# Kernel optimization log

Hardware: AMD Instinct MI355X
Metric: run time of the kernel (lower is better)

The kernel has to match this reference:

```python
import jax, jax.numpy as jnp
import numpy as np


def _cofactor_antieq(M):
    """ith output = M[...,i,0] * (-1)**i * det(M with row i and col 0 deleted).

    M: (..., n, n) -> (..., n). Vectorized form of the original per-row
    jnp.delete + stack + det construction.
    """
    n = M.shape[-1]
    # rows[i] = all row indices except i, shape (n, n-1)
    rows = np.stack([np.delete(np.arange(n), i) for i in range(n)])
    Msub = M[..., 1:]                 # delete first column: (..., n, n-1)
    sub = Msub[..., rows, :]          # delete row i per output: (..., n, n-1, n-1)
    signs = jnp.asarray((-1.0) ** np.arange(n), dtype=M.dtype)
    return M[..., 0] * signs * jnp.linalg.det(sub)


def setup_inputs() -> dict:
    key = jax.random.key(0)
    ks = jax.random.split(key, 6)
    B, NSPIN, NPS, D, NION, DIM = 4096, 2, 16, 256, 8, 3
    eq_inputs = jax.random.normal(ks[0], (B, NSPIN * NPS, D), jnp.float32)
    r_ei = jax.random.normal(ks[1], (B, NSPIN * NPS, NION, DIM), jnp.float32)
    # per-spin linear orbital params (stacked over spin since splits are equal)
    W = jax.random.normal(ks[2], (NSPIN, D, NPS), jnp.float32) / np.sqrt(D)
    b = jax.random.normal(ks[3], (NSPIN, NPS), jnp.float32) * 0.01
    # anisotropic envelope decay matrices A per (spin, ion, orbital), near identity
    env_dim = jax.random.normal(ks[4], (NSPIN, NION, NPS, DIM, DIM), jnp.float32) * 0.1 + jnp.eye(DIM, dtype=jnp.float32)
    # linear combination over ions per (spin, orbital)
    env_ion = jax.random.normal(ks[5], (NSPIN, NION, NPS), jnp.float32) / NION
    return dict(eq_inputs=eq_inputs, r_ei=r_ei, W=W, b=b, env_dim=env_dim, env_ion=env_ion)


def reference(eq_inputs, r_ei, W, b, env_dim, env_ion):
    B = eq_inputs.shape[0]
    nspin, d, nps = W.shape
    nion, dim = r_ei.shape[-2], r_ei.shape[-1]
    # split particles by spin: (B, nspin, nps, ...)
    xs = eq_inputs.reshape(B, nspin, nps, d)
    rs = r_ei.reshape(B, nspin, nps, nion, dim)
    # linear part of orbitals: (B, s, n, o) with n = o = nps (square per spin)
    y = jnp.einsum('bsnd,sdo->bsno', xs, W) + b[:, None, :]
    # anisotropic exponential envelope: exp(-||A (r - R)||), summed over ions
    Ar = jnp.einsum('sioed,bsnid->bsnioe', env_dim, rs)        # (B,s,n,ion,orb,3)
    env = jnp.einsum('bsnio,sio->bsno',
                     jnp.exp(-jnp.linalg.norm(Ar, axis=-1)), env_ion)
    M = y * env                                                 # (B, s, n, n)
    cof = _cofactor_antieq(M)                                   # (B, s, n)
    return cof[..., None]                                       # (B, s, n, 1)
```

## Files before the change

### kernel.cpp

```cpp
#include <hip/hip_runtime.h>
#include <math.h>


__global__ __launch_bounds__(256)
void cof_fused(const float* __restrict__ eq,
               const float* __restrict__ rei,
               const float* __restrict__ Wm,
               const float* __restrict__ bb,
               const float* __restrict__ edim,
               const float* __restrict__ eion,
               float* __restrict__ out)
{
  __shared__ __align__(16) float Gl[8 * 6 * 16];
  __shared__ __align__(16) float Ml[4 * 328];

  const int tid   = threadIdx.x;
  const int lane  = tid & 63;
  const int wv    = tid >> 6;
  const int blk   = blockIdx.x;
  const int sp    = blk >> 10;
  const int bbase = (blk & 1023) * 4;

  if (tid < 128) {
    const int i = tid >> 4, o = tid & 15;
    const float* A = edim + (((size_t)sp * 8 + i) * 16 + o) * 9;
    const float a0=A[0],a1=A[1],a2=A[2],a3=A[3],a4=A[4],a5=A[5],a6=A[6],a7=A[7],a8=A[8];
    float* Gp = Gl + i * 96 + o;
    Gp[0]  = a0*a0 + a3*a3 + a6*a6;
    Gp[16] = a1*a1 + a4*a4 + a7*a7;
    Gp[32] = a2*a2 + a5*a5 + a8*a8;
    Gp[48] = 2.f*(a0*a1 + a3*a4 + a6*a7);
    Gp[64] = 2.f*(a0*a2 + a3*a5 + a6*a8);
    Gp[80] = 2.f*(a1*a2 + a4*a5 + a7*a8);
  }
  __syncthreads();

  const int bidx = bbase + wv;
  const int cch  = lane >> 4;
  const int nb   = (lane >> 2) & 3;
  const int ob   = lane & 3;

  const float* xb = eq + ((size_t)bidx * 32 + sp * 16) * 256;
  const float* wb = Wm + (size_t)sp * 4096;

  float acc[4][4] = {{0.f,0.f,0.f,0.f},{0.f,0.f,0.f,0.f},
                     {0.f,0.f,0.f,0.f},{0.f,0.f,0.f,0.f}};
  #pragma unroll 2
  for (int q = 0; q < 16; ++q) {
    const int d0 = cch * 64 + q * 4;
    float xr[4][4], wr[4][4];
    #pragma unroll
    for (int r = 0; r < 4; ++r) {
      float4 t = *(const float4*)(xb + (4 * nb + r) * 256 + d0);
      xr[r][0]=t.x; xr[r][1]=t.y; xr[r][2]=t.z; xr[r][3]=t.w;
    }
    #pragma unroll
    for (int j = 0; j < 4; ++j) {
      float4 t = *(const float4*)(wb + (d0 + j) * 16 + 4 * ob);
      wr[j][0]=t.x; wr[j][1]=t.y; wr[j][2]=t.z; wr[j][3]=t.w;
    }
    #pragma unroll
    for (int r = 0; r < 4; ++r)
      #pragma unroll
      for (int j = 0; j < 4; ++j)
        #pragma unroll
        for (int c2 = 0; c2 < 4; ++c2)
          acc[r][c2] = fmaf(xr[r][j], wr[j][c2], acc[r][c2]);
  }

  #pragma unroll
  for (int r = 0; r < 4; ++r)
    #pragma unroll
    for (int c2 = 0; c2 < 4; ++c2) {
      float v = acc[r][c2];
      v += __shfl_xor(v, 16);
      v += __shfl_xor(v, 32);
      acc[r][c2] = v;
    }

  {
    float4 bv = *(const float4*)(bb + sp * 16 + 4 * ob);
    if (lane < 16) {
      #pragma unroll
      for (int r = 0; r < 4; ++r) {
        float4 v = make_float4(acc[r][0] + bv.x, acc[r][1] + bv.y,
                               acc[r][2] + bv.z, acc[r][3] + bv.w);
        *(float4*)(Ml + wv * 328 + (4 * nb + r) * 20 + 4 * ob) = v;
      }
    }
  }
  __syncthreads();

  {
    const int n = lane >> 2;
    const float* rp = rei + ((size_t)bidx * 32 + sp * 16 + n) * 24;
    float rv[24];
    #pragma unroll
    for (int t4 = 0; t4 < 6; ++t4) {
      float4 t = *(const float4*)(rp + t4 * 4);
      rv[t4*4+0]=t.x; rv[t4*4+1]=t.y; rv[t4*4+2]=t.z; rv[t4*4+3]=t.w;
    }
    float4 env = make_float4(0.f, 0.f, 0.f, 0.f);
    #pragma unroll
    for (int i = 0; i < 8; ++i) {
      const float r0 = rv[i*3], r1 = rv[i*3+1], r2 = rv[i*3+2];
      const float rr0 = r0*r0, rr1 = r1*r1, rr2 = r2*r2;
      const float rr3 = r0*r1, rr4 = r0*r2, rr5 = r1*r2;
      const float* Gp = Gl + i * 96 + 4 * ob;
      const float4 q00 = *(const float4*)(Gp);
      const float4 q11 = *(const float4*)(Gp + 16);
      const float4 q22 = *(const float4*)(Gp + 32);
      const float4 q01 = *(const float4*)(Gp + 48);
      const float4 q02 = *(const float4*)(Gp + 64);
      const float4 q12 = *(const float4*)(Gp + 80);
      const float4 io  = *(const float4*)(eion + ((size_t)sp * 8 + i) * 16 + 4 * ob);
#define ENVC(c) { float n2 = q00.c*rr0 + q11.c*rr1 + q22.c*rr2 \
                           + q01.c*rr3 + q02.c*rr4 + q12.c*rr5; \
                  n2 = fmaxf(n2, 0.f); \
                  env.c += expf(-sqrtf(n2)) * io.c; }
      ENVC(x) ENVC(y) ENVC(z) ENVC(w)
#undef ENVC
    }
    float* mp = Ml + wv * 328 + n * 20 + 4 * ob;
    float4 y = *(const float4*)mp;
    *(float4*)mp = make_float4(y.x * env.x, y.y * env.y, y.z * env.z, y.w * env.w);
  }
  __syncthreads();

  if (wv == 0) {
    const int g  = lane >> 4;
    const int r  = lane & 15;
    const int gb = lane & 48;
    const float* mg = Ml + g * 328;
    float a[16];
    #pragma unroll
    for (int c = 0; c < 16; ++c) a[c] = mg[c * 20 + r];

    float det = 1.0f;
    int sign = 0;
    unsigned retired = 0;
    int piv[16];
    int srr = 0;
    float accf = (r == 0) ? 1.0f : 0.0f;
    float acc2 = 0.0f;

    #pragma unroll
    for (int k = 0; k < 16; ++k) {
      const bool act = ((retired >> r) & 1u) == 0u;
      const float av = act ? fabsf(a[k]) : 0.0f;
      unsigned pk = (__float_as_uint(av) & 0xFFFFFFF0u) | (unsigned)r;
      #pragma unroll
      for (int m = 1; m <= 8; m <<= 1) {
        unsigned o2 = __shfl_xor(pk, m);
        pk = (pk > o2) ? pk : o2;
      }
      const int p = (int)(pk & 15u);
      piv[k] = p;
      float pv = __shfl(a[k], gb | p);
      if (fabsf(pv) < 1e-30f) pv = (pv < 0.0f) ? -1e-30f : 1e-30f;
      det *= pv;
      retired |= (1u << p);
      sign ^= (int)(__popc((~retired) & ((1u << p) - 1u)) & 1u);
      if (r == p) srr = k;
      const bool upd = act && (r != p);
      float m2 = 0.0f;
      if (upd) { m2 = a[k] / pv; a[k] = m2; }
      #pragma unroll
      for (int c = k + 1; c < 16; ++c) {
        float bcv = __shfl(a[c], gb | p);
        if (upd) a[c] = fmaf(-m2, bcv, a[c]);
      }
      float zk = __shfl(accf, gb | p);
      if (r == p) acc2 = zk;
      if (upd) accf = fmaf(-m2, zk, accf);
    }
    if (sign) det = -det;

    float myx = 0.0f;
    #pragma unroll
    for (int j = 15; j >= 0; --j) {
      float t = acc2 / a[j];
      float xj = __shfl(t, gb | piv[j]);
      if (srr < j) acc2 = fmaf(-a[j], xj, acc2);
      if (r == j) myx = xj;
    }

    const float mi0 = mg[r * 20];
    const float cof = mi0 * det * myx;
    out[((size_t)(bbase + g) * 2 + sp) * 16 + r] = cof;
  }
}

extern "C" void kernel_launch(void* const* d_in, const int* in_sizes, int n_in,
                              void* d_out, int out_size, void* d_ws, size_t ws_size,
                              hipStream_t stream) {
  (void)in_sizes; (void)n_in; (void)out_size; (void)d_ws; (void)ws_size;
  const float* eq   = (const float*)d_in[0];
  const float* rei  = (const float*)d_in[1];
  const float* Wm   = (const float*)d_in[2];
  const float* bb   = (const float*)d_in[3];
  const float* edim = (const float*)d_in[4];
  const float* eion = (const float*)d_in[5];
  float* out = (float*)d_out;
  hipLaunchKernelGGL(cof_fused, dim3(2048), dim3(256), 0, stream,
                     eq, rei, Wm, bb, edim, eion, out);
}
```

Baseline: 239.8 us.

## Stage eq rows through swizzled LDS with register prefetch, drop a barrier

Each wavefront now loads its 16x256 slice of eq_inputs with coalesced float4 loads into a per-wave LDS buffer, in two 128-column halves. The LDS writes use an XOR swizzle, and the second half is prefetched into registers while the first half is consumed. The GEMM then reads x from LDS instead of making strided global loads, and the reduction split across channel groups is interleaved rather than blocked. The M matrix reuses the same per-wave buffer, which allows removing one block-wide barrier, and expf is replaced by the faster __expf. This raises LDS use to about 33KB per block, which may limit occupancy, and __expf slightly reduces accuracy.

New measurement: 230.3 us. -4.0%, faster.

```diff
diff --git a/kernel.cpp b/kernel.cpp
--- a/kernel.cpp
+++ b/kernel.cpp
@@ -12,7 +12,7 @@
                float* __restrict__ out)
 {
   __shared__ __align__(16) float Gl[8 * 6 * 16];
-  __shared__ __align__(16) float Ml[4 * 328];
+  __shared__ __align__(16) float Xl[4 * 2048];
 
   const int tid   = threadIdx.x;
   const int lane  = tid & 63;
@@ -42,16 +42,65 @@
 
   const float* xb = eq + ((size_t)bidx * 32 + sp * 16) * 256;
   const float* wb = Wm + (size_t)sp * 4096;
+  float* xw = Xl + wv * 2048;
+
+  const int srow = 2 * 0 + (lane >> 5);
+  const int schk = lane & 31;
 
   float acc[4][4] = {{0.f,0.f,0.f,0.f},{0.f,0.f,0.f,0.f},
                      {0.f,0.f,0.f,0.f},{0.f,0.f,0.f,0.f}};
+
+  float4 st[8];
+  #pragma unroll
+  for (int t = 0; t < 8; ++t)
+    st[t] = *(const float4*)(xb + (2 * t + (lane >> 5)) * 256 + schk * 4);
+  #pragma unroll
+  for (int t = 0; t < 8; ++t) {
+    const int row = 2 * t + (lane >> 5);
+    *(float4*)(xw + row * 128 + (schk ^ (row & 7)) * 4) = st[t];
+  }
+  float4 st2[8];
+  #pragma unroll
+  for (int t = 0; t < 8; ++t)
+    st2[t] = *(const float4*)(xb + (2 * t + (lane >> 5)) * 256 + 128 + schk * 4);
+
   #pragma unroll 2
-  for (int q = 0; q < 16; ++q) {
-    const int d0 = cch * 64 + q * 4;
+  for (int q = 0; q < 8; ++q) {
+    const int d0 = q * 16 + cch * 4;
     float xr[4][4], wr[4][4];
     #pragma unroll
     for (int r = 0; r < 4; ++r) {
-      float4 t = *(const float4*)(xb + (4 * nb + r) * 256 + d0);
+      const int n = 4 * nb + r;
+      float4 t = *(const float4*)(xw + n * 128 + ((q * 4 + cch) ^ (n & 7)) * 4);
+      xr[r][0]=t.x; xr[r][1]=t.y; xr[r][2]=t.z; xr[r][3]=t.w;
+    }
+    #pragma unroll
+    for (int j = 0; j < 4; ++j) {
+      float4 t = *(const float4*)(wb + (d0 + j) * 16 + 4 * ob);
+      wr[j][0]=t.x; wr[j][1]=t.y; wr[j][2]=t.z; wr[j][3]=t.w;
+    }
+    #pragma unroll
+    for (int r = 0; r < 4; ++r)
+      #pragma unroll
+      for (int j = 0; j < 4; ++j)
+        #pragma unroll
+        for (int c2 = 0; c2 < 4; ++c2)
+          acc[r][c2] = fmaf(xr[r][j], wr[j][c2], acc[r][c2]);
+  }
+
+  #pragma unroll
+  for (int t = 0; t < 8; ++t) {
+    const int row = 2 * t + (lane >> 5);
+    *(float4*)(xw + row * 128 + (schk ^ (row & 7)) * 4) = st2[t];
+  }
+  #pragma unroll 2
+  for (int q = 0; q < 8; ++q) {
+    const int d0 = 128 + q * 16 + cch * 4;
+    float xr[4][4], wr[4][4];
+    #pragma unroll
+    for (int r = 0; r < 4; ++r) {
+      const int n = 4 * nb + r;
+      float4 t = *(const float4*)(xw + n * 128 + ((q * 4 + cch) ^ (n & 7)) * 4);
       xr[r][0]=t.x; xr[r][1]=t.y; xr[r][2]=t.z; xr[r][3]=t.w;
     }
     #pragma unroll
@@ -78,6 +127,7 @@
       acc[r][c2] = v;
     }
 
+  float* Mw = xw;
   {
     float4 bv = *(const float4*)(bb + sp * 16 + 4 * ob);
     if (lane < 16) {
@@ -85,11 +135,10 @@
       for (int r = 0; r < 4; ++r) {
         float4 v = make_float4(acc[r][0] + bv.x, acc[r][1] + bv.y,
                                acc[r][2] + bv.z, acc[r][3] + bv.w);
-        *(float4*)(Ml + wv * 328 + (4 * nb + r) * 20 + 4 * ob) = v;
+        *(float4*)(Mw + (4 * nb + r) * 20 + 4 * ob) = v;
       }
     }
   }
-  __syncthreads();
 
   {
     const int n = lane >> 2;
@@ -117,11 +166,11 @@
 #define ENVC(c) { float n2 = q00.c*rr0 + q11.c*rr1 + q22.c*rr2 \
                            + q01.c*rr3 + q02.c*rr4 + q12.c*rr5; \
                   n2 = fmaxf(n2, 0.f); \
-                  env.c += expf(-sqrtf(n2)) * io.c; }
+                  env.c += __expf(-sqrtf(n2)) * io.c; }
       ENVC(x) ENVC(y) ENVC(z) ENVC(w)
 #undef ENVC
     }
-    float* mp = Ml + wv * 328 + n * 20 + 4 * ob;
+    float* mp = Mw + n * 20 + 4 * ob;
     float4 y = *(const float4*)mp;
     *(float4*)mp = make_float4(y.x * env.x, y.y * env.y, y.z * env.z, y.w * env.w);
   }
@@ -131,7 +180,7 @@
     const int g  = lane >> 4;
     const int r  = lane & 15;
     const int gb = lane & 48;
-    const float* mg = Ml + g * 328;
+    const float* mg = Xl + g * 2048;
     float a[16];
     #pragma unroll
     for (int c = 0; c < 16; ++c) a[c] = mg[c * 20 + r];
```

## Stage X through swizzled LDS, make each wave independent, use fast exp

Applied to the files above, without the earlier changes.

Each wave now copies its 16x256 input rows into a per-wave, XOR-swizzled LDS buffer in coalesced chunks before the GEMM inner loop. The orbital-matrix scratch reuses that buffer, and the block-wide barriers after the GEMM and envelope stages are removed. Each wave then runs its own 16-lane LU and cofactor solve instead of leaving wave 0 to do all four batches, so waves no longer wait on each other. It also uses __expf, packs pivot indices into a 64-bit integer to avoid a local array, and sets launch_bounds(256, 8). That occupancy target may cap registers tightly enough to cause spills.

Measured after the change: 283.2 us. 18.1% more time.

```diff
diff --git a/kernel.cpp b/kernel.cpp
--- a/kernel.cpp
+++ b/kernel.cpp
@@ -2,7 +2,7 @@
 #include <math.h>
 
 
-__global__ __launch_bounds__(256)
+__global__ __launch_bounds__(256, 8)
 void cof_fused(const float* __restrict__ eq,
                const float* __restrict__ rei,
                const float* __restrict__ Wm,
@@ -12,7 +12,7 @@
                float* __restrict__ out)
 {
   __shared__ __align__(16) float Gl[8 * 6 * 16];
-  __shared__ __align__(16) float Ml[4 * 328];
+  __shared__ __align__(16) float Xl[4 * 1024];
 
   const int tid   = threadIdx.x;
   const int lane  = tid & 63;
@@ -42,30 +42,44 @@
 
   const float* xb = eq + ((size_t)bidx * 32 + sp * 16) * 256;
   const float* wb = Wm + (size_t)sp * 4096;
+  float* xw = Xl + wv * 1024;
+
+  const int srow = lane >> 4;
+  const int scol = lane & 15;
 
   float acc[4][4] = {{0.f,0.f,0.f,0.f},{0.f,0.f,0.f,0.f},
                      {0.f,0.f,0.f,0.f},{0.f,0.f,0.f,0.f}};
-  #pragma unroll 2
-  for (int q = 0; q < 16; ++q) {
-    const int d0 = cch * 64 + q * 4;
-    float xr[4][4], wr[4][4];
-    #pragma unroll
-    for (int r = 0; r < 4; ++r) {
-      float4 t = *(const float4*)(xb + (4 * nb + r) * 256 + d0);
-      xr[r][0]=t.x; xr[r][1]=t.y; xr[r][2]=t.z; xr[r][3]=t.w;
-    }
-    #pragma unroll
-    for (int j = 0; j < 4; ++j) {
-      float4 t = *(const float4*)(wb + (d0 + j) * 16 + 4 * ob);
-      wr[j][0]=t.x; wr[j][1]=t.y; wr[j][2]=t.z; wr[j][3]=t.w;
-    }
-    #pragma unroll
-    for (int r = 0; r < 4; ++r)
-      #pragma unroll
-      for (int j = 0; j < 4; ++j)
+
+  for (int c = 0; c < 4; ++c) {
+    #pragma unroll
+    for (int t = 0; t < 4; ++t) {
+      const int row = 4 * t + srow;
+      float4 v = *(const float4*)(xb + row * 256 + c * 64 + scol * 4);
+      *(float4*)(xw + row * 64 + (scol ^ (row & 7)) * 4) = v;
+    }
+    #pragma unroll
+    for (int q = 0; q < 4; ++q) {
+      const int d0 = c * 64 + q * 16 + cch * 4;
+      float xr[4][4], wr[4][4];
+      #pragma unroll
+      for (int r = 0; r < 4; ++r) {
+        const int n = 4 * nb + r;
+        float4 t = *(const float4*)(xw + n * 64 + (((q * 4 + cch) ^ (n & 7))) * 4);
+        xr[r][0]=t.x; xr[r][1]=t.y; xr[r][2]=t.z; xr[r][3]=t.w;
+      }
+      #pragma unroll
+      for (int j = 0; j < 4; ++j) {
+        float4 t = *(const float4*)(wb + (d0 + j) * 16 + 4 * ob);
+        wr[j][0]=t.x; wr[j][1]=t.y; wr[j][2]=t.z; wr[j][3]=t.w;
+      }
+      #pragma unroll
+      for (int r = 0; r < 4; ++r)
         #pragma unroll
-        for (int c2 = 0; c2 < 4; ++c2)
-          acc[r][c2] = fmaf(xr[r][j], wr[j][c2], acc[r][c2]);
+        for (int j = 0; j < 4; ++j)
+          #pragma unroll
+          for (int c2 = 0; c2 < 4; ++c2)
+            acc[r][c2] = fmaf(xr[r][j], wr[j][c2], acc[r][c2]);
+    }
   }
 
   #pragma unroll
@@ -78,6 +92,7 @@
       acc[r][c2] = v;
     }
 
+  float* Mw = xw;
   {
     float4 bv = *(const float4*)(bb + sp * 16 + 4 * ob);
     if (lane < 16) {
@@ -85,11 +100,10 @@
       for (int r = 0; r < 4; ++r) {
         float4 v = make_float4(acc[r][0] + bv.x, acc[r][1] + bv.y,
                                acc[r][2] + bv.z, acc[r][3] + bv.w);
-        *(float4*)(Ml + wv * 328 + (4 * nb + r) * 20 + 4 * ob) = v;
-      }
-    }
-  }
-  __syncthreads();
+        *(float4*)(Mw + (4 * nb + r) * 20 + 4 * ob) = v;
+      }
+    }
+  }
 
   {
     const int n = lane >> 2;
@@ -117,29 +131,25 @@
 #define ENVC(c) { float n2 = q00.c*rr0 + q11.c*rr1 + q22.c*rr2 \
                            + q01.c*rr3 + q02.c*rr4 + q12.c*rr5; \
                   n2 = fmaxf(n2, 0.f); \
-                  env.c += expf(-sqrtf(n2)) * io.c; }
+                  env.c += __expf(-sqrtf(n2)) * io.c; }
       ENVC(x) ENVC(y) ENVC(z) ENVC(w)
 #undef ENVC
     }
-    float* mp = Ml + wv * 328 + n * 20 + 4 * ob;
+    float* mp = Mw + n * 20 + 4 * ob;
     float4 y = *(const float4*)mp;
     *(float4*)mp = make_float4(y.x * env.x, y.y * env.y, y.z * env.z, y.w * env.w);
   }
-  __syncthreads();
-
-  if (wv == 0) {
-    const int g  = lane >> 4;
-    const int r  = lane & 15;
-    const int gb = lane & 48;
-    const float* mg = Ml + g * 328;
+
+  if (lane < 16) {
+    const int r = lane;
     float a[16];
     #pragma unroll
-    for (int c = 0; c < 16; ++c) a[c] = mg[c * 20 + r];
+    for (int c = 0; c < 16; ++c) a[c] = Mw[c * 20 + r];
 
     float det = 1.0f;
     int sign = 0;
     unsigned retired = 0;
-    int piv[16];
+    unsigned long long pivpack = 0ull;
     int srr = 0;
     float accf = (r == 0) ? 1.0f : 0.0f;
     float acc2 = 0.0f;
@@ -155,8 +165,8 @@
         pk = (pk > o2) ? pk : o2;
       }
       const int p = (int)(pk & 15u);
-      piv[k] = p;
-      float pv = __shfl(a[k], gb | p);
+      pivpack |= (unsigned long long)(unsigned)p << (4 * k);
+      float pv = __shfl(a[k], p);
       if (fabsf(pv) < 1e-30f) pv = (pv < 0.0f) ? -1e-30f : 1e-30f;
       det *= pv;
       retired |= (1u << p);
@@ -167,10 +177,10 @@
       if (upd) { m2 = a[k] / pv; a[k] = m2; }
       #pragma unroll
       for (int c = k + 1; c < 16; ++c) {
-        float bcv = __shfl(a[c], gb | p);
+        float bcv = __shfl(a[c], p);
         if (upd) a[c] = fmaf(-m2, bcv, a[c]);
       }
-      float zk = __shfl(accf, gb | p);
+      float zk = __shfl(accf, p);
       if (r == p) acc2 = zk;
       if (upd) accf = fmaf(-m2, zk, accf);
     }
@@ -179,15 +189,16 @@
     float myx = 0.0f;
     #pragma unroll
     for (int j = 15; j >= 0; --j) {
+      const int pj = (int)((pivpack >> (4 * j)) & 15ull);
       float t = acc2 / a[j];
-      float xj = __shfl(t, gb | piv[j]);
+      float xj = __shfl(t, pj);
       if (srr < j) acc2 = fmaf(-a[j], xj, acc2);
       if (r == j) myx = xj;
     }
 
-    const float mi0 = mg[r * 20];
+    const float mi0 = Mw[r * 20];
     const float cof = mi0 * det * myx;
-    out[((size_t)(bbase + g) * 2 + sp) * 16 + r] = cof;
+    out[((size_t)bidx * 2 + sp) * 16 + r] = cof;
   }
 }
 
```
